# Kernel optimization log

Measured on AMD Instinct MI355X. Metric: run time of the kernel, lower is better.

Reference implementation:

```python
import jax, jax.numpy as jnp
import numpy as np

EMBED_DIM = 768
NUM_HEADS = 12
HEAD_DIM = EMBED_DIM // NUM_HEADS
BS, SEQ = 2, 2048
NEG_BIG = -1e20  # matches torch masked_fill value


def setup_inputs() -> dict:
    key = jax.random.key(0)
    ks = jax.random.split(key, 8)
    Q = jax.random.normal(ks[0], (BS, SEQ, EMBED_DIM), dtype=jnp.float32)
    K = jax.random.normal(ks[1], (BS, SEQ, EMBED_DIM), dtype=jnp.float32)
    V = jax.random.normal(ks[2], (BS, SEQ, EMBED_DIM), dtype=jnp.float32)
    mask = jax.random.randint(ks[3], (1, 1, SEQ, SEQ), 0, 2, dtype=jnp.int32)
    scale = 1.0 / np.sqrt(EMBED_DIM).astype(np.float32)
    Wq = jax.random.normal(ks[4], (EMBED_DIM, EMBED_DIM), dtype=jnp.float32) * 0.02
    Wk = jax.random.normal(ks[5], (EMBED_DIM, EMBED_DIM), dtype=jnp.float32) * 0.02
    Wv = jax.random.normal(ks[6], (EMBED_DIM, EMBED_DIM), dtype=jnp.float32) * 0.02
    Wo = jax.random.normal(ks[7], (EMBED_DIM, EMBED_DIM), dtype=jnp.float32) * 0.02
    return {"Q": Q, "K": K, "V": V, "mask": mask,
            "Wq": Wq, "Wk": Wk, "Wv": Wv, "Wo": Wo}


def reference(Q, K, V, mask, Wq, Wk, Wv, Wo):
    bs, q_len, D = Q.shape
    H, hd = NUM_HEADS, HEAD_DIM
    # QKV projections (nn.Linear, no bias): x @ W.T
    q = (Q @ Wq.T).reshape(bs, q_len, H, hd)            # nqhd
    k = (K @ Wk.T).reshape(bs, K.shape[1], H, hd)       # nkhd
    v = (V @ Wv.T).reshape(bs, V.shape[1], H, hd)       # nlhd
    # unfused attention, faithful to source (scale by sqrt(embed_dim)!)
    energy = jnp.einsum('nqhd,nkhd->nhqk', q, k)
    energy = jnp.where(mask == 0, jnp.float32(NEG_BIG), energy)
    attn = jax.nn.softmax(energy * (1.0 / jnp.sqrt(jnp.float32(D))), axis=3)
    out = jnp.einsum('nhql,nlhd->nqhd', attn, v).reshape(bs, q_len, H * hd)
    return out @ Wo.T
```

## Files before the change

### kernel.cpp

```cpp
#include <hip/hip_runtime.h>
#include <cmath>

typedef __bf16 bf16x8 __attribute__((ext_vector_type(8)));
typedef float f32x4 __attribute__((ext_vector_type(4)));
typedef unsigned int u32x4 __attribute__((ext_vector_type(4)));

#define SEQ 2048
#define EMBED 768
#define NHEAD 12
#define HDIM 64
#define NTOK 4096
#define NBH 24
#define NSPLIT 4
#define TILES_PER_SPLIT (SEQ / 64 / NSPLIT)
#define SCALE_LOG2 (1.4426950408889634f * 0.036084391824351615f)
#define NEGBIG2 (-5.205878509564917e18f)

__device__ __forceinline__ void gload_lds16(const __bf16* g, __bf16* l) {
  __builtin_amdgcn_global_load_lds(
      (const __attribute__((address_space(1))) void*)g,
      (__attribute__((address_space(3))) void*)l, 16, 0, 0);
}

__device__ __forceinline__ unsigned pack2(float a, float b) {
  unsigned short lo = __builtin_bit_cast(unsigned short, (__bf16)a);
  unsigned short hi = __builtin_bit_cast(unsigned short, (__bf16)b);
  return (unsigned)lo | ((unsigned)hi << 16);
}

__global__ __launch_bounds__(256) void cvt_qkv(const float* __restrict__ Q,
                                               const float* __restrict__ K,
                                               const float* __restrict__ V,
                                               __bf16* __restrict__ Qb,
                                               __bf16* __restrict__ Kb,
                                               __bf16* __restrict__ Vb) {
  const float* s = blockIdx.y == 0 ? Q : blockIdx.y == 1 ? K : V;
  __bf16* d = blockIdx.y == 0 ? Qb : blockIdx.y == 1 ? Kb : Vb;
  size_t i = ((size_t)blockIdx.x * 256 + threadIdx.x) * 8;
  float4 a = *(const float4*)(s + i);
  float4 c = *(const float4*)(s + i + 4);
  bf16x8 r;
  r[0] = (__bf16)a.x; r[1] = (__bf16)a.y; r[2] = (__bf16)a.z; r[3] = (__bf16)a.w;
  r[4] = (__bf16)c.x; r[5] = (__bf16)c.y; r[6] = (__bf16)c.z; r[7] = (__bf16)c.w;
  *(bf16x8*)(d + i) = r;
}

__global__ __launch_bounds__(256) void cvt_w(const float* __restrict__ W0,
                                             const float* __restrict__ W1,
                                             const float* __restrict__ W2,
                                             const float* __restrict__ W3,
                                             __bf16* __restrict__ O0,
                                             __bf16* __restrict__ O1,
                                             __bf16* __restrict__ O2,
                                             __bf16* __restrict__ O3) {
  const float* s = blockIdx.y == 0 ? W0 : blockIdx.y == 1 ? W1 : blockIdx.y == 2 ? W2 : W3;
  __bf16* d = blockIdx.y == 0 ? O0 : blockIdx.y == 1 ? O1 : blockIdx.y == 2 ? O2 : O3;
  size_t i = ((size_t)blockIdx.x * 256 + threadIdx.x) * 8;
  float4 a = *(const float4*)(s + i);
  float4 c = *(const float4*)(s + i + 4);
  bf16x8 r;
  r[0] = (__bf16)a.x; r[1] = (__bf16)a.y; r[2] = (__bf16)a.z; r[3] = (__bf16)a.w;
  r[4] = (__bf16)c.x; r[5] = (__bf16)c.y; r[6] = (__bf16)c.z; r[7] = (__bf16)c.w;
  *(bf16x8*)(d + i) = r;
}

__global__ __launch_bounds__(256) void pack_mask_k(const int* __restrict__ mask,
                                                   unsigned long long* __restrict__ bits) {
  int e = blockIdx.x * 256 + threadIdx.x;
  unsigned long long b = __ballot(mask[e] != 0);
  if ((threadIdx.x & 63) == 0) bits[e >> 6] = b;
}

template <int MODE, typename CT>
__device__ __forceinline__ void gemm_body(const __bf16* __restrict__ A,
                                          const __bf16* __restrict__ B,
                                          CT* __restrict__ C, int N, int row0,
                                          int col0, float alpha, __bf16* As,
                                          __bf16* Bs) {
  const int K = EMBED;
  const int tid = threadIdx.x;
  const int lane = tid & 63;
  const int wave = tid >> 6;
  const int wr = wave >> 1, wc = wave & 1;
  const int l15 = lane & 15, g = lane >> 4;
  f32x4 acc[4][4] = {};

  const int srow = tid >> 3;
  const int scol8 = (tid & 7) ^ (srow & 7);
  const __bf16* aS = A + (size_t)(row0 + srow) * K + scol8 * 8;
  const __bf16* bS = B + (size_t)(col0 + srow) * K + scol8 * 8;
  __bf16* aL = As + wave * 512;
  __bf16* bL = Bs + wave * 512;

  for (int k0 = 0; k0 < K; k0 += 64) {
    __syncthreads();
#pragma unroll
    for (int q = 0; q < 4; ++q) {
      gload_lds16(aS + k0 + (size_t)(q * 32) * K, aL + q * 2048);
      gload_lds16(bS + k0 + (size_t)(q * 32) * K, bL + q * 2048);
    }
    __syncthreads();
    bf16x8 af[2][4], bfr[2][4];
#pragma unroll
    for (int i = 0; i < 4; ++i) {
      int row = wr * 64 + i * 16 + l15;
#pragma unroll
      for (int kk = 0; kk < 2; ++kk)
        af[kk][i] =
            *(const bf16x8*)(As + row * 64 + ((kk * 4 + g) ^ (row & 7)) * 8);
    }
#pragma unroll
    for (int j = 0; j < 4; ++j) {
      int row = wc * 64 + j * 16 + l15;
#pragma unroll
      for (int kk = 0; kk < 2; ++kk)
        bfr[kk][j] =
            *(const bf16x8*)(Bs + row * 64 + ((kk * 4 + g) ^ (row & 7)) * 8);
    }
#pragma unroll
    for (int kk = 0; kk < 2; ++kk)
#pragma unroll
      for (int i = 0; i < 4; ++i)
#pragma unroll
        for (int j = 0; j < 4; ++j)
          acc[i][j] = __builtin_amdgcn_mfma_f32_16x16x32_bf16(
              af[kk][i], bfr[kk][j], acc[i][j], 0, 0, 0);
  }
#pragma unroll
  for (int i = 0; i < 4; ++i)
#pragma unroll
    for (int j = 0; j < 4; ++j) {
#pragma unroll
      for (int r = 0; r < 4; ++r) {
        float val = alpha * acc[i][j][r];
        int mrow = row0 + wr * 64 + i * 16 + g * 4 + r;
        int ncol = col0 + wc * 64 + j * 16 + l15;
        if (MODE == 0 || MODE == 3) {
          C[(size_t)mrow * N + ncol] = (CT)val;
        } else if (MODE == 1) {
          int tok = mrow, fcol = ncol;
          int h = fcol >> 6, d = fcol & 63;
          int bh = (tok >> 11) * NHEAD + h;
          int t = (tok >> 6) & 31, kk = tok & 63;
          size_t idx = ((size_t)bh * 32 + t) * 4096 +
                       ((((kk >> 4) * 2 + (d >> 5)) * 64 + ((d >> 3) & 3) * 16 +
                         (kk & 15)) *
                            8 +
                        (d & 7));
          C[idx] = (CT)val;
        } else {
          int fr = mrow, tok = ncol;
          int h = fr >> 6, d = fr & 63;
          int dt = d >> 4, l15c = d & 15;
          int bh = (tok >> 11) * NHEAD + h;
          int t = (tok >> 6) & 31, kk = tok & 63;
          int pc = (kk & 32) | ((kk & 12) << 1) | ((kk & 16) >> 2) | (kk & 3);
          int ks = pc >> 5, Gb = (pc >> 3) & 3, e = pc & 7;
          size_t idx = ((size_t)bh * 32 + t) * 4096 +
                       (((ks * 4 + dt) * 64 + Gb * 16 + l15c) * 8 + e);
          C[idx] = (CT)val;
        }
      }
    }
}

__global__ __launch_bounds__(256) void gemm_qkv(
    const __bf16* __restrict__ Qb, const __bf16* __restrict__ Kb,
    const __bf16* __restrict__ Vb, const __bf16* __restrict__ Wqb,
    const __bf16* __restrict__ Wkb, const __bf16* __restrict__ Wvb,
    __bf16* __restrict__ qh, __bf16* __restrict__ khF, __bf16* __restrict__ vTF) {
  __shared__ __align__(16) __bf16 As[128 * 64];
  __shared__ __align__(16) __bf16 Bs[128 * 64];
  if (blockIdx.z == 0)
    gemm_body<0, __bf16>(Qb, Wqb, qh, EMBED, blockIdx.x * 128,
                         blockIdx.y * 128, SCALE_LOG2, As, Bs);
  else if (blockIdx.z == 1)
    gemm_body<1, __bf16>(Kb, Wkb, khF, 0, blockIdx.x * 128, blockIdx.y * 128,
                         1.f, As, Bs);
  else
    gemm_body<2, __bf16>(Wvb, Vb, vTF, 0, blockIdx.y * 128, blockIdx.x * 128,
                         1.f, As, Bs);
}

__global__ __launch_bounds__(256) void gemm_out(const __bf16* __restrict__ AO,
                                                const __bf16* __restrict__ Wob,
                                                float* __restrict__ out) {
  __shared__ __align__(16) __bf16 As[128 * 64];
  __shared__ __align__(16) __bf16 Bs[128 * 64];
  gemm_body<3, float>(AO, Wob, out, EMBED, blockIdx.x * 128, blockIdx.y * 128,
                      1.f, As, Bs);
}

__global__ __launch_bounds__(256, 4) void flash_attn(
    const __bf16* __restrict__ qh, const __bf16* __restrict__ khF,
    const __bf16* __restrict__ vTF, const unsigned long long* __restrict__ mbits,
    float* __restrict__ Opart, float* __restrict__ lpart) {
  __shared__ __align__(16) __bf16 Ks[4096];
  __shared__ __align__(16) __bf16 Vs[4096];
  int lin = blockIdx.x + 16 * (blockIdx.y + NBH * blockIdx.z);
  int wid = (lin & 7) * 192 + (lin >> 3);
  int qb = wid & 15;
  int rest = wid >> 4;
  int bh = rest % NBH;
  int z = rest / NBH;

  const int tid = threadIdx.x;
  const int lane = tid & 63, w = tid >> 6;
  const int l15 = lane & 15, G = lane >> 4;
  const int b = bh / NHEAD, h = bh % NHEAD;
  const int qrow0 = qb * 128 + w * 32;

  bf16x8 qf[2][2];
#pragma unroll
  for (int qg = 0; qg < 2; ++qg) {
    const __bf16* qptr =
        qh + ((size_t)b * SEQ + qrow0 + qg * 16 + l15) * EMBED + h * HDIM + G * 8;
    qf[qg][0] = *(const bf16x8*)qptr;
    qf[qg][1] = *(const bf16x8*)(qptr + 32);
  }
  const u32x4 onesr = {0x3F803F80u, 0x3F803F80u, 0x3F803F80u, 0x3F803F80u};
  const bf16x8 ones = __builtin_bit_cast(bf16x8, onesr);

  f32x4 o[2][4] = {};
  f32x4 ol[2] = {};

  const __bf16* ktile =
      khF + ((size_t)bh * 32 + z * TILES_PER_SPLIT) * 4096 + tid * 8;
  const __bf16* vtile =
      vTF + ((size_t)bh * 32 + z * TILES_PER_SPLIT) * 4096 + tid * 8;
  const unsigned long long* mrow0 =
      mbits + (size_t)(qrow0 + l15) * 32 + z * TILES_PER_SPLIT;
  const unsigned long long* mrow1 = mrow0 + 16 * 32;

  for (int tt = 0; tt < TILES_PER_SPLIT; ++tt) {
    __syncthreads();
    gload_lds16(ktile, Ks + w * 512);
    gload_lds16(ktile + 2048, Ks + w * 512 + 2048);
    gload_lds16(vtile, Vs + w * 512);
    gload_lds16(vtile + 2048, Vs + w * 512 + 2048);
    ktile += 4096;
    vtile += 4096;
    unsigned long long mb0 = mrow0[tt], mb1 = mrow1[tt];
    __syncthreads();

    f32x4 s[2][4];
#pragma unroll
    for (int jj = 0; jj < 4; ++jj) {
      bf16x8 kf0 = *(const bf16x8*)(Ks + (jj * 2 + 0) * 512 + lane * 8);
      bf16x8 kf1 = *(const bf16x8*)(Ks + (jj * 2 + 1) * 512 + lane * 8);
#pragma unroll
      for (int qg = 0; qg < 2; ++qg) {
        f32x4 zz = {};
        zz = __builtin_amdgcn_mfma_f32_16x16x32_bf16(kf0, qf[qg][0], zz, 0, 0, 0);
        zz = __builtin_amdgcn_mfma_f32_16x16x32_bf16(kf1, qf[qg][1], zz, 0, 0, 0);
        s[qg][jj] = zz;
      }
    }
    unsigned pfw[2][2][4];
#pragma unroll
    for (int qg = 0; qg < 2; ++qg) {
      unsigned long long mb = qg == 0 ? mb0 : mb1;
      unsigned mlo = ((unsigned)mb) >> (G * 4);
      unsigned mhi = ((unsigned)(mb >> 32)) >> (G * 4);
#pragma unroll
      for (int jj = 0; jj < 4; ++jj) {
        unsigned bits = (jj < 2 ? mlo : mhi) >> ((jj & 1) * 16);
#pragma unroll
        for (int r = 0; r < 4; ++r) {
          float val = ((bits >> r) & 1u) ? s[qg][jj][r] : NEGBIG2;
          s[qg][jj][r] = __builtin_amdgcn_exp2f(val);
        }
      }
#pragma unroll
      for (int ks = 0; ks < 2; ++ks) {
        pfw[qg][ks][0] = pack2(s[qg][2 * ks][0], s[qg][2 * ks][1]);
        pfw[qg][ks][1] = pack2(s[qg][2 * ks][2], s[qg][2 * ks][3]);
        pfw[qg][ks][2] = pack2(s[qg][2 * ks + 1][0], s[qg][2 * ks + 1][1]);
        pfw[qg][ks][3] = pack2(s[qg][2 * ks + 1][2], s[qg][2 * ks + 1][3]);
      }
    }
#pragma unroll
    for (int ks = 0; ks < 2; ++ks) {
      u32x4 p0 = {pfw[0][ks][0], pfw[0][ks][1], pfw[0][ks][2], pfw[0][ks][3]};
      u32x4 p1 = {pfw[1][ks][0], pfw[1][ks][1], pfw[1][ks][2], pfw[1][ks][3]};
      bf16x8 pf0 = __builtin_bit_cast(bf16x8, p0);
      bf16x8 pf1 = __builtin_bit_cast(bf16x8, p1);
      ol[0] = __builtin_amdgcn_mfma_f32_16x16x32_bf16(ones, pf0, ol[0], 0, 0, 0);
      ol[1] = __builtin_amdgcn_mfma_f32_16x16x32_bf16(ones, pf1, ol[1], 0, 0, 0);
#pragma unroll
      for (int dt = 0; dt < 4; ++dt) {
        bf16x8 vf = *(const bf16x8*)(Vs + (ks * 4 + dt) * 512 + lane * 8);
        o[0][dt] = __builtin_amdgcn_mfma_f32_16x16x32_bf16(vf, pf0, o[0][dt], 0, 0, 0);
        o[1][dt] = __builtin_amdgcn_mfma_f32_16x16x32_bf16(vf, pf1, o[1][dt], 0, 0, 0);
      }
    }
  }
#pragma unroll
  for (int qg = 0; qg < 2; ++qg) {
    int qrow = qrow0 + qg * 16 + l15;
    size_t obase = (((size_t)z * NBH + bh) * SEQ + qrow) * HDIM;
    f32x4* op = (f32x4*)(Opart + obase);
#pragma unroll
    for (int dt = 0; dt < 4; ++dt) op[dt * 4 + G] = o[qg][dt];
    if (G == 0)
      lpart[((size_t)z * NBH + bh) * SEQ + qrow] = ol[qg][0];
  }
}

__global__ __launch_bounds__(256) void combine(const float* __restrict__ Opart,
                                               const float* __restrict__ lpart,
                                               __bf16* __restrict__ AO) {
  int idx = blockIdx.x * 256 + threadIdx.x;
  int bhq = idx >> 4, dq = idx & 15;
  int bh = bhq >> 11, q = bhq & (SEQ - 1);
  const f32x4* Ov = (const f32x4*)Opart;
  float lsum = 0.f;
  float r0 = 0.f, r1 = 0.f, r2 = 0.f, r3 = 0.f;
#pragma unroll
  for (int s = 0; s < NSPLIT; ++s) {
    lsum += lpart[(size_t)s * NBH * SEQ + bhq];
    f32x4 a = Ov[(size_t)s * NBH * SEQ * 16 + (size_t)bhq * 16 + dq];
    r0 += a[0];
    r1 += a[1];
    r2 += a[2];
    r3 += a[3];
  }
  float inv = 1.f / lsum;
  int bb = bh / NHEAD, hh = bh % NHEAD;
  unsigned* dst =
      (unsigned*)(AO + ((size_t)bb * SEQ + q) * EMBED + hh * HDIM + dq * 4);
  dst[0] = pack2(r0 * inv, r1 * inv);
  dst[1] = pack2(r2 * inv, r3 * inv);
}

extern "C" void kernel_launch(void* const* d_in, const int* in_sizes, int n_in,
                              void* d_out, int out_size, void* d_ws,
                              size_t ws_size, hipStream_t stream) {
  const float* Q = (const float*)d_in[0];
  const float* K = (const float*)d_in[1];
  const float* V = (const float*)d_in[2];
  const int* mask = (const int*)d_in[3];
  const float* Wq = (const float*)d_in[4];
  const float* Wk = (const float*)d_in[5];
  const float* Wv = (const float*)d_in[6];
  const float* Wo = (const float*)d_in[7];
  float* out = (float*)d_out;

  char* ws = (char*)d_ws;
  const size_t ACT = (size_t)NTOK * EMBED * 2;
  const size_t WMT = (size_t)EMBED * EMBED * 2;
  const size_t OPART_B = (size_t)NSPLIT * NBH * SEQ * HDIM * 4;

  float* Opart = (float*)ws;
  __bf16* Qb = (__bf16*)ws;
  __bf16* Kb = (__bf16*)(ws + ACT);
  __bf16* Vb = (__bf16*)(ws + 2 * ACT);
  __bf16* Wqb = (__bf16*)(ws + 3 * ACT);
  __bf16* Wkb = (__bf16*)(ws + 3 * ACT + WMT);
  __bf16* Wvb = (__bf16*)(ws + 3 * ACT + 2 * WMT);
  size_t off = OPART_B;
  auto alloc = [&](size_t bytes) {
    char* p = ws + off;
    off += (bytes + 255) & ~(size_t)255;
    return p;
  };
  __bf16* Wob = (__bf16*)alloc(WMT);
  __bf16* qh = (__bf16*)alloc(ACT);
  __bf16* khF = (__bf16*)alloc(ACT);
  __bf16* vTF = (__bf16*)alloc(ACT);
  __bf16* AO = (__bf16*)alloc(ACT);
  unsigned long long* mbits =
      (unsigned long long*)alloc((size_t)SEQ * (SEQ / 64) * 8);
  float* lpart = (float*)alloc((size_t)NSPLIT * NBH * SEQ * 4);

  cvt_qkv<<<dim3(NTOK * EMBED / 2048, 3), 256, 0, stream>>>(Q, K, V, Qb, Kb, Vb);
  cvt_w<<<dim3(EMBED * EMBED / 2048, 4), 256, 0, stream>>>(Wq, Wk, Wv, Wo, Wqb,
                                                           Wkb, Wvb, Wob);
  pack_mask_k<<<dim3(SEQ * SEQ / 256), 256, 0, stream>>>(mask, mbits);
  gemm_qkv<<<dim3(NTOK / 128, EMBED / 128, 3), 256, 0, stream>>>(
      Qb, Kb, Vb, Wqb, Wkb, Wvb, qh, khF, vTF);
  flash_attn<<<dim3(SEQ / 128, NBH, NSPLIT), 256, 0, stream>>>(qh, khF, vTF,
                                                               mbits, Opart,
                                                               lpart);
  combine<<<dim3(NBH * SEQ * 16 / 256), 256, 0, stream>>>(Opart, lpart, AO);
  gemm_out<<<dim3(NTOK / 128, EMBED / 128), 256, 0, stream>>>(AO, Wob, out);
  (void)in_sizes; (void)n_in; (void)out_size; (void)ws_size;
}
```

Before: 124.2 us.

## Double-buffer LDS in GEMMs and flash attention, halve KV splits, mask after exp

Both the GEMM body and the flash-attention loop now double-buffer their LDS tiles, issuing the next tile's global-to-LDS loads before computing on the current one. A single wait-then-barrier replaces the two syncthreads per iteration, and s_setprio raises wave priority around the MFMA sections. The KV split count drops from 4 to 2, so there are fewer partial outputs to combine but each block runs longer. Masking now ANDs the exp2 result with a sign-extended mask bit instead of selecting a large negative input, at the cost of doubled LDS use, which may reduce occupancy.

```diff
diff --git a/kernel.cpp b/kernel.cpp
--- a/kernel.cpp
+++ b/kernel.cpp
@@ -11,10 +11,9 @@
 #define HDIM 64
 #define NTOK 4096
 #define NBH 24
-#define NSPLIT 4
+#define NSPLIT 2
 #define TILES_PER_SPLIT (SEQ / 64 / NSPLIT)
 #define SCALE_LOG2 (1.4426950408889634f * 0.036084391824351615f)
-#define NEGBIG2 (-5.205878509564917e18f)
 
 __device__ __forceinline__ void gload_lds16(const __bf16* g, __bf16* l) {
   __builtin_amdgcn_global_load_lds(
@@ -26,6 +25,12 @@
   unsigned short lo = __builtin_bit_cast(unsigned short, (__bf16)a);
   unsigned short hi = __builtin_bit_cast(unsigned short, (__bf16)b);
   return (unsigned)lo | ((unsigned)hi << 16);
+}
+
+__device__ __forceinline__ void phase_barrier() {
+  asm volatile("s_waitcnt vmcnt(0)" ::: "memory");
+  __builtin_amdgcn_s_barrier();
+  __builtin_amdgcn_sched_barrier(0);
 }
 
 __global__ __launch_bounds__(256) void cvt_qkv(const float* __restrict__ Q,
@@ -78,6 +83,7 @@
                                           int col0, float alpha, __bf16* As,
                                           __bf16* Bs) {
   const int K = EMBED;
+  const int NIT = K / 64;
   const int tid = threadIdx.x;
   const int lane = tid & 63;
   const int wave = tid >> 6;
@@ -92,14 +98,22 @@
   __bf16* aL = As + wave * 512;
   __bf16* bL = Bs + wave * 512;
 
-  for (int k0 = 0; k0 < K; k0 += 64) {
-    __syncthreads();
+  auto stage = [&](int buf, int k0) {
 #pragma unroll
     for (int q = 0; q < 4; ++q) {
-      gload_lds16(aS + k0 + (size_t)(q * 32) * K, aL + q * 2048);
-      gload_lds16(bS + k0 + (size_t)(q * 32) * K, bL + q * 2048);
-    }
-    __syncthreads();
+      gload_lds16(aS + k0 + (size_t)(q * 32) * K, aL + buf * 8192 + q * 2048);
+      gload_lds16(bS + k0 + (size_t)(q * 32) * K, bL + buf * 8192 + q * 2048);
+    }
+  };
+
+  stage(0, 0);
+#pragma unroll 2
+  for (int it = 0; it < NIT; ++it) {
+    const int c = it & 1;
+    phase_barrier();
+    if (it + 1 < NIT) stage(1 - c, (it + 1) * 64);
+    const __bf16* Asc = As + c * 8192;
+    const __bf16* Bsc = Bs + c * 8192;
     bf16x8 af[2][4], bfr[2][4];
 #pragma unroll
     for (int i = 0; i < 4; ++i) {
@@ -107,7 +121,7 @@
 #pragma unroll
       for (int kk = 0; kk < 2; ++kk)
         af[kk][i] =
-            *(const bf16x8*)(As + row * 64 + ((kk * 4 + g) ^ (row & 7)) * 8);
+            *(const bf16x8*)(Asc + row * 64 + ((kk * 4 + g) ^ (row & 7)) * 8);
     }
 #pragma unroll
     for (int j = 0; j < 4; ++j) {
@@ -115,8 +129,9 @@
 #pragma unroll
       for (int kk = 0; kk < 2; ++kk)
         bfr[kk][j] =
-            *(const bf16x8*)(Bs + row * 64 + ((kk * 4 + g) ^ (row & 7)) * 8);
-    }
+            *(const bf16x8*)(Bsc + row * 64 + ((kk * 4 + g) ^ (row & 7)) * 8);
+    }
+    __builtin_amdgcn_s_setprio(1);
 #pragma unroll
     for (int kk = 0; kk < 2; ++kk)
 #pragma unroll
@@ -125,6 +140,7 @@
         for (int j = 0; j < 4; ++j)
           acc[i][j] = __builtin_amdgcn_mfma_f32_16x16x32_bf16(
               af[kk][i], bfr[kk][j], acc[i][j], 0, 0, 0);
+    __builtin_amdgcn_s_setprio(0);
   }
 #pragma unroll
   for (int i = 0; i < 4; ++i)
@@ -169,8 +185,8 @@
     const __bf16* __restrict__ Vb, const __bf16* __restrict__ Wqb,
     const __bf16* __restrict__ Wkb, const __bf16* __restrict__ Wvb,
     __bf16* __restrict__ qh, __bf16* __restrict__ khF, __bf16* __restrict__ vTF) {
-  __shared__ __align__(16) __bf16 As[128 * 64];
-  __shared__ __align__(16) __bf16 Bs[128 * 64];
+  __shared__ __align__(16) __bf16 As[2 * 128 * 64];
+  __shared__ __align__(16) __bf16 Bs[2 * 128 * 64];
   if (blockIdx.z == 0)
     gemm_body<0, __bf16>(Qb, Wqb, qh, EMBED, blockIdx.x * 128,
                          blockIdx.y * 128, SCALE_LOG2, As, Bs);
@@ -185,8 +201,8 @@
 __global__ __launch_bounds__(256) void gemm_out(const __bf16* __restrict__ AO,
                                                 const __bf16* __restrict__ Wob,
                                                 float* __restrict__ out) {
-  __shared__ __align__(16) __bf16 As[128 * 64];
-  __shared__ __align__(16) __bf16 Bs[128 * 64];
+  __shared__ __align__(16) __bf16 As[2 * 128 * 64];
+  __shared__ __align__(16) __bf16 Bs[2 * 128 * 64];
   gemm_body<3, float>(AO, Wob, out, EMBED, blockIdx.x * 128, blockIdx.y * 128,
                       1.f, As, Bs);
 }
@@ -195,10 +211,10 @@
     const __bf16* __restrict__ qh, const __bf16* __restrict__ khF,
     const __bf16* __restrict__ vTF, const unsigned long long* __restrict__ mbits,
     float* __restrict__ Opart, float* __restrict__ lpart) {
-  __shared__ __align__(16) __bf16 Ks[4096];
-  __shared__ __align__(16) __bf16 Vs[4096];
+  __shared__ __align__(16) __bf16 Ks[2][4096];
+  __shared__ __align__(16) __bf16 Vs[2][4096];
   int lin = blockIdx.x + 16 * (blockIdx.y + NBH * blockIdx.z);
-  int wid = (lin & 7) * 192 + (lin >> 3);
+  int wid = (lin & 7) * 96 + (lin >> 3);
   int qb = wid & 15;
   int rest = wid >> 4;
   int bh = rest % NBH;
@@ -232,22 +248,36 @@
       mbits + (size_t)(qrow0 + l15) * 32 + z * TILES_PER_SPLIT;
   const unsigned long long* mrow1 = mrow0 + 16 * 32;
 
+  gload_lds16(ktile, &Ks[0][0] + w * 512);
+  gload_lds16(ktile + 2048, &Ks[0][0] + w * 512 + 2048);
+  gload_lds16(vtile, &Vs[0][0] + w * 512);
+  gload_lds16(vtile + 2048, &Vs[0][0] + w * 512 + 2048);
+  unsigned long long mb0 = mrow0[0], mb1 = mrow1[0];
+
+#pragma unroll 2
   for (int tt = 0; tt < TILES_PER_SPLIT; ++tt) {
-    __syncthreads();
-    gload_lds16(ktile, Ks + w * 512);
-    gload_lds16(ktile + 2048, Ks + w * 512 + 2048);
-    gload_lds16(vtile, Vs + w * 512);
-    gload_lds16(vtile + 2048, Vs + w * 512 + 2048);
-    ktile += 4096;
-    vtile += 4096;
-    unsigned long long mb0 = mrow0[tt], mb1 = mrow1[tt];
-    __syncthreads();
+    const int c = tt & 1;
+    phase_barrier();
+    unsigned long long nmb0 = 0, nmb1 = 0;
+    if (tt + 1 < TILES_PER_SPLIT) {
+      const __bf16* kt = ktile + (size_t)(tt + 1) * 4096;
+      const __bf16* vt = vtile + (size_t)(tt + 1) * 4096;
+      __bf16* kd = &Ks[1 - c][0] + w * 512;
+      __bf16* vd = &Vs[1 - c][0] + w * 512;
+      gload_lds16(kt, kd);
+      gload_lds16(kt + 2048, kd + 2048);
+      gload_lds16(vt, vd);
+      gload_lds16(vt + 2048, vd + 2048);
+      nmb0 = mrow0[tt + 1];
+      nmb1 = mrow1[tt + 1];
+    }
 
     f32x4 s[2][4];
+    __builtin_amdgcn_s_setprio(1);
 #pragma unroll
     for (int jj = 0; jj < 4; ++jj) {
-      bf16x8 kf0 = *(const bf16x8*)(Ks + (jj * 2 + 0) * 512 + lane * 8);
-      bf16x8 kf1 = *(const bf16x8*)(Ks + (jj * 2 + 1) * 512 + lane * 8);
+      bf16x8 kf0 = *(const bf16x8*)(&Ks[c][0] + (jj * 2 + 0) * 512 + lane * 8);
+      bf16x8 kf1 = *(const bf16x8*)(&Ks[c][0] + (jj * 2 + 1) * 512 + lane * 8);
 #pragma unroll
       for (int qg = 0; qg < 2; ++qg) {
         f32x4 zz = {};
@@ -256,6 +286,8 @@
         s[qg][jj] = zz;
       }
     }
+    __builtin_amdgcn_s_setprio(0);
+
     unsigned pfw[2][2][4];
 #pragma unroll
     for (int qg = 0; qg < 2; ++qg) {
@@ -267,8 +299,10 @@
         unsigned bits = (jj < 2 ? mlo : mhi) >> ((jj & 1) * 16);
 #pragma unroll
         for (int r = 0; r < 4; ++r) {
-          float val = ((bits >> r) & 1u) ? s[qg][jj][r] : NEGBIG2;
-          s[qg][jj][r] = __builtin_amdgcn_exp2f(val);
+          float p = __builtin_amdgcn_exp2f(s[qg][jj][r]);
+          int sm = ((int)(bits << (31 - r))) >> 31;
+          s[qg][jj][r] = __builtin_bit_cast(
+              float, __builtin_bit_cast(unsigned, p) & (unsigned)sm);
         }
       }
 #pragma unroll
@@ -279,6 +313,7 @@
         pfw[qg][ks][3] = pack2(s[qg][2 * ks + 1][2], s[qg][2 * ks + 1][3]);
       }
     }
+    __builtin_amdgcn_s_setprio(1);
 #pragma unroll
     for (int ks = 0; ks < 2; ++ks) {
       u32x4 p0 = {pfw[0][ks][0], pfw[0][ks][1], pfw[0][ks][2], pfw[0][ks][3]};
@@ -289,11 +324,14 @@
       ol[1] = __builtin_amdgcn_mfma_f32_16x16x32_bf16(ones, pf1, ol[1], 0, 0, 0);
 #pragma unroll
       for (int dt = 0; dt < 4; ++dt) {
-        bf16x8 vf = *(const bf16x8*)(Vs + (ks * 4 + dt) * 512 + lane * 8);
+        bf16x8 vf = *(const bf16x8*)(&Vs[c][0] + (ks * 4 + dt) * 512 + lane * 8);
         o[0][dt] = __builtin_amdgcn_mfma_f32_16x16x32_bf16(vf, pf0, o[0][dt], 0, 0, 0);
         o[1][dt] = __builtin_amdgcn_mfma_f32_16x16x32_bf16(vf, pf1, o[1][dt], 0, 0, 0);
       }
     }
+    __builtin_amdgcn_s_setprio(0);
+    mb0 = nmb0;
+    mb1 = nmb1;
   }
 #pragma unroll
   for (int qg = 0; qg < 2; ++qg) {
```

Result: faster. 116.8 us (-6.0%).
